# Kernel tuning notes

Hardware: AMD Instinct MI355X
Metric: run time of the kernel (lower is better)

The kernel has to match this reference:

```python
import jax, jax.numpy as jnp
import numpy as np

N_HEAD = 16
N_STATE = 1024
NEG_INF = -1e9


def setup_inputs() -> dict:
    key = jax.random.key(0)
    k1, = jax.random.split(key, 1)
    B, S = 4, 2048
    x = jax.random.normal(k1, (B, S, 3 * N_STATE), dtype=jnp.float32)
    # causal attention mask (1 = keep, 0 = masked), broadcast over heads
    attn_mask = jnp.tril(jnp.ones((S, S), dtype=jnp.float32))[None, None, :, :]
    attn_mask = jnp.broadcast_to(attn_mask, (B, 1, S, S))
    return {"x": x, "attn_mask": attn_mask}


def reference(x, attn_mask) -> jnp.ndarray:
    B, S, _ = x.shape
    d_head = N_STATE // N_HEAD
    q = x[:, :, :N_STATE].reshape(B, S, N_HEAD, d_head).transpose(0, 2, 1, 3)  # [B,H,S,D]
    k = x[:, :, N_STATE:2 * N_STATE].reshape(B, S, N_HEAD, d_head).transpose(0, 2, 1, 3)
    v = x[:, :, 2 * N_STATE:].reshape(B, S, N_HEAD, d_head).transpose(0, 2, 1, 3)
    scale = 1.0 / jnp.sqrt(jnp.asarray(d_head, dtype=x.dtype))
    w = jnp.einsum('bhqd,bhkd->bhqk', q, k) * scale           # [B,H,S,S]
    w = attn_mask * w + (1.0 - attn_mask) * NEG_INF
    w = jax.nn.softmax(w, axis=-1)
    # attention_dropout is identity at inference (Keras Dropout, training=False)
    a = jnp.einsum('bhqk,bhkd->bhqd', w, v)                   # [B,H,S,D]
    return a.transpose(0, 2, 1, 3).reshape(B, S, N_STATE)
```

## Files before the change

### kernel.cpp

```cpp
#include <hip/hip_runtime.h>


typedef float  f32x4  __attribute__((ext_vector_type(4)));
typedef short  bf16x8 __attribute__((ext_vector_type(8)));

#define NH      16
#define DH      64
#define SEQ     2048
#define NSTATE  1024
#define ROW3    3072
#define BQ      128
#define BK      64
#define NQB     (SEQ / BQ)
#define KST     72
#define VST     72
#define PST     72
#define NEG_BIG (-1e9f)
#define QSC     (0.125f * 1.4426950408889634f)

static __device__ __forceinline__ unsigned pk2(float x, float y) {
    unsigned ux = __builtin_bit_cast(unsigned, x);
    unsigned uy = __builtin_bit_cast(unsigned, y);
    ux += 0x7FFFu + ((ux >> 16) & 1u);
    uy += 0x7FFFu + ((uy >> 16) & 1u);
    return __builtin_amdgcn_perm(uy, ux, 0x07060302u);
}

#define ISSUE_STAGE(KV0)                                                       \
    {                                                                          \
        _Pragma("unroll")                                                      \
        for (int i = 0; i < 2; ++i) {                                          \
            int p  = tid + 512 * i;                                            \
            int kv = p >> 4;                                                   \
            int d  = (p & 15) * 4;                                             \
            kp[i] = *(const float4*)(kbase + (size_t)((KV0) + kv) * ROW3 + d); \
        }                                                                      \
        _Pragma("unroll")                                                      \
        for (int i = 0; i < 4; ++i) {                                          \
            int idx = tid + 512 * i;                                           \
            int d   = idx & 63;                                                \
            int kv  = (idx >> 6) * 2;                                          \
            const float* gp = vbase + (size_t)((KV0) + kv) * ROW3 + d;         \
            vp[2 * i]     = gp[0];                                             \
            vp[2 * i + 1] = gp[ROW3];                                          \
        }                                                                      \
    }

#define COMMIT_STAGE(BUF)                                                      \
    {                                                                          \
        _Pragma("unroll")                                                      \
        for (int i = 0; i < 2; ++i) {                                          \
            int p  = tid + 512 * i;                                            \
            int kv = p >> 4;                                                   \
            int d  = (p & 15) * 4;                                             \
            uint2 w;                                                           \
            w.x = pk2(kp[i].x, kp[i].y);                                       \
            w.y = pk2(kp[i].z, kp[i].w);                                       \
            *(uint2*)&Klds[BUF][kv * KST + d] = w;                             \
        }                                                                      \
        _Pragma("unroll")                                                      \
        for (int i = 0; i < 4; ++i) {                                          \
            int idx = tid + 512 * i;                                           \
            int d   = idx & 63;                                                \
            int kv  = (idx >> 6) * 2;                                          \
            *(unsigned*)&Vlds[BUF][d * VST + kv] = pk2(vp[2 * i], vp[2 * i + 1]); \
        }                                                                      \
    }

__global__ __launch_bounds__(512, 4)
void mha_fwd(const float* __restrict__ x, float* __restrict__ out) {
    const int tid  = threadIdx.x;
    const int wave = tid >> 6;
    const int lane = tid & 63;
    const int l16  = lane & 15;
    const int quad = lane >> 4;

    const int pr = blockIdx.x;
    const int bh = blockIdx.y;
    const int b  = bh >> 4;
    const int h  = bh & 15;

    const float* xb    = x + (size_t)b * SEQ * ROW3;
    const float* kbase = xb + NSTATE + h * DH;
    const float* vbase = xb + 2 * NSTATE + h * DH;
    float*       ob    = out + (size_t)b * SEQ * NSTATE + h * DH;

    __shared__ __align__(16) short Klds[2][BK * KST];
    __shared__ __align__(16) short Vlds[2][DH * VST];
    __shared__ __align__(16) short Plds[8][16 * PST];

    bf16x8 vones;
#pragma unroll
    for (int i = 0; i < 8; ++i) vones[i] = (short)0x3F80;

    float4 kp[2];
    float  vp[8];

#pragma unroll 1
    for (int ph = 0; ph < 2; ++ph) {
        const int qblk = ph ? (NQB - 1 - pr) : pr;
        const int q0   = qblk * BQ;
        const int qmin = q0 + wave * 16;
        const int qrow = qmin + l16;

        bf16x8 qf[2];
        {
            const float* qp = xb + (size_t)qrow * ROW3 + h * DH + quad * 8;
#pragma unroll
            for (int f = 0; f < 2; ++f) {
                float4 a = *(const float4*)(qp + 32 * f);
                float4 c = *(const float4*)(qp + 32 * f + 4);
                union { bf16x8 v; unsigned u[4]; } qq;
                qq.u[0] = pk2(a.x * QSC, a.y * QSC);
                qq.u[1] = pk2(a.z * QSC, a.w * QSC);
                qq.u[2] = pk2(c.x * QSC, c.y * QSC);
                qq.u[3] = pk2(c.z * QSC, c.w * QSC);
                qf[f] = qq.v;
            }
        }

        f32x4 o[4];
#pragma unroll
        for (int t = 0; t < 4; ++t) o[t] = (f32x4){0.f, 0.f, 0.f, 0.f};
        f32x4 ol = (f32x4){0.f, 0.f, 0.f, 0.f};

        const int ntiles = q0 / BK + BQ / BK;

        __syncthreads();
        ISSUE_STAGE(0)
        COMMIT_STAGE(0)
        __syncthreads();

#pragma unroll 1
        for (int it = 0; it < ntiles; ++it) {
            const int kv0 = it * BK;
            const int cur = it & 1;
            const bool pf = (it + 1 < ntiles);

            if (pf) ISSUE_STAGE((it + 1) * BK)

            if (kv0 <= qmin + 15) {
                bf16x8 kf[4][2];
#pragma unroll
                for (int t = 0; t < 4; ++t)
#pragma unroll
                    for (int f = 0; f < 2; ++f)
                        kf[t][f] = *(const bf16x8*)&Klds[cur][(16 * t + l16) * KST + quad * 8 + 32 * f];
                bf16x8 vf[4][2];
#pragma unroll
                for (int t = 0; t < 4; ++t)
#pragma unroll
                    for (int f = 0; f < 2; ++f)
                        vf[t][f] = *(const bf16x8*)&Vlds[cur][(16 * t + l16) * VST + quad * 8 + 32 * f];

                f32x4 sc[4];
#pragma unroll
                for (int t = 0; t < 4; ++t) {
                    f32x4 c = (f32x4){0.f, 0.f, 0.f, 0.f};
                    c = __builtin_amdgcn_mfma_f32_16x16x32_bf16(kf[t][0], qf[0], c, 0, 0, 0);
                    c = __builtin_amdgcn_mfma_f32_16x16x32_bf16(kf[t][1], qf[1], c, 0, 0, 0);
                    sc[t] = c;
                }
                if (kv0 + BK - 1 > qmin) {
#pragma unroll
                    for (int t = 0; t < 4; ++t)
#pragma unroll
                        for (int r = 0; r < 4; ++r) {
                            int kvg = kv0 + 16 * t + 4 * quad + r;
                            if (kvg > qrow) sc[t][r] = NEG_BIG;
                        }
                }

#pragma unroll
                for (int t = 0; t < 4; ++t)
#pragma unroll
                    for (int r = 0; r < 4; ++r)
                        sc[t][r] = __builtin_amdgcn_exp2f(sc[t][r]);

                short* pb = &Plds[wave][0];
#pragma unroll
                for (int t = 0; t < 4; ++t) {
                    uint2 pk;
                    pk.x = pk2(sc[t][0], sc[t][1]);
                    pk.y = pk2(sc[t][2], sc[t][3]);
                    *(uint2*)&pb[l16 * PST + 16 * t + 4 * quad] = pk;
                }
                __asm__ volatile("s_waitcnt lgkmcnt(0)" ::: "memory");
                bf16x8 pf0 = *(const bf16x8*)&pb[l16 * PST + quad * 8];
                bf16x8 pf1 = *(const bf16x8*)&pb[l16 * PST + quad * 8 + 32];

#pragma unroll
                for (int t = 0; t < 4; ++t) {
                    f32x4 c = o[t];
                    c = __builtin_amdgcn_mfma_f32_16x16x32_bf16(pf0, vf[t][0], c, 0, 0, 0);
                    c = __builtin_amdgcn_mfma_f32_16x16x32_bf16(pf1, vf[t][1], c, 0, 0, 0);
                    o[t] = c;
                }
                ol = __builtin_amdgcn_mfma_f32_16x16x32_bf16(pf0, vones, ol, 0, 0, 0);
                ol = __builtin_amdgcn_mfma_f32_16x16x32_bf16(pf1, vones, ol, 0, 0, 0);
            }

            if (pf) COMMIT_STAGE(cur ^ 1)
            __syncthreads();
        }

        {
            const int qtop = qmin + 4 * quad;
            float lr[4];
#pragma unroll
            for (int r = 0; r < 4; ++r) lr[r] = 1.0f / ol[r];
#pragma unroll
            for (int t = 0; t < 4; ++t)
#pragma unroll
                for (int r = 0; r < 4; ++r)
                    ob[(size_t)(qtop + r) * NSTATE + 16 * t + l16] = o[t][r] * lr[r];
        }
    }
}

extern "C" void kernel_launch(void* const* d_in, const int* in_sizes, int n_in,
                              void* d_out, int out_size, void* d_ws, size_t ws_size,
                              hipStream_t stream) {
    const float* x = (const float*)d_in[0];
    float* out = (float*)d_out;
    dim3 grid(NQB / 2, 4 * NH);
    dim3 block(512);
    hipLaunchKernelGGL(mha_fwd, grid, block, 0, stream, x, out);
}
```

Measured before the change: 252.7 us.

## Switch attention to 32x32x16 MFMA with register-resident P and larger Q tiles

Replaces the 16x16x32 MFMA tiles with 32x32x16 MFMAs, so each wave owns a 32-row query strip and the query block grows to 256. The P matrix is now repacked in registers with v_permlane32_swap instead of going through an LDS round trip. The row sum is accumulated with VALU adds rather than an extra ones-MFMA, and the grid is flattened so blocks sharing a query block are grouped by head. In exchange, the larger tiles raise register pressure and the launch bounds drop to 2 blocks per SM. With only 4 paired blocks per head, there are fewer workgroups overall.

After: 219.1 us. -13.3%, faster.

```diff
diff --git a/kernel.cpp b/kernel.cpp
--- a/kernel.cpp
+++ b/kernel.cpp
@@ -1,20 +1,20 @@
 #include <hip/hip_runtime.h>
 
 
-typedef float  f32x4  __attribute__((ext_vector_type(4)));
-typedef short  bf16x8 __attribute__((ext_vector_type(8)));
+typedef float  f32x4   __attribute__((ext_vector_type(4)));
+typedef float  f32x16  __attribute__((ext_vector_type(16)));
+typedef short  bf16x8  __attribute__((ext_vector_type(8)));
 
 #define NH      16
 #define DH      64
 #define SEQ     2048
 #define NSTATE  1024
 #define ROW3    3072
-#define BQ      128
+#define BQ      256
 #define BK      64
 #define NQB     (SEQ / BQ)
 #define KST     72
 #define VST     72
-#define PST     72
 #define NEG_BIG (-1e9f)
 #define QSC     (0.125f * 1.4426950408889634f)
 
@@ -33,13 +33,12 @@
             int p  = tid + 512 * i;                                            \
             int kv = p >> 4;                                                   \
             int d  = (p & 15) * 4;                                             \
-            kp[i] = *(const float4*)(kbase + (size_t)((KV0) + kv) * ROW3 + d); \
+            kp[i] = *(const f32x4*)(kbase + (size_t)((KV0) + kv) * ROW3 + d);  \
         }                                                                      \
         _Pragma("unroll")                                                      \
         for (int i = 0; i < 4; ++i) {                                          \
-            int idx = tid + 512 * i;                                           \
-            int d   = idx & 63;                                                \
-            int kv  = (idx >> 6) * 2;                                          \
+            int d  = (tid & 15) + 16 * i;                                      \
+            int kv = (tid >> 4) * 2;                                           \
             const float* gp = vbase + (size_t)((KV0) + kv) * ROW3 + d;         \
             vp[2 * i]     = gp[0];                                             \
             vp[2 * i + 1] = gp[ROW3];                                          \
@@ -54,31 +53,31 @@
             int kv = p >> 4;                                                   \
             int d  = (p & 15) * 4;                                             \
             uint2 w;                                                           \
-            w.x = pk2(kp[i].x, kp[i].y);                                       \
-            w.y = pk2(kp[i].z, kp[i].w);                                       \
+            w.x = pk2(kp[i][0], kp[i][1]);                                     \
+            w.y = pk2(kp[i][2], kp[i][3]);                                     \
             *(uint2*)&Klds[BUF][kv * KST + d] = w;                             \
         }                                                                      \
         _Pragma("unroll")                                                      \
         for (int i = 0; i < 4; ++i) {                                          \
-            int idx = tid + 512 * i;                                           \
-            int d   = idx & 63;                                                \
-            int kv  = (idx >> 6) * 2;                                          \
+            int d  = (tid & 15) + 16 * i;                                      \
+            int kv = (tid >> 4) * 2;                                           \
             *(unsigned*)&Vlds[BUF][d * VST + kv] = pk2(vp[2 * i], vp[2 * i + 1]); \
         }                                                                      \
     }
 
-__global__ __launch_bounds__(512, 4)
+__global__ __launch_bounds__(512, 2)
 void mha_fwd(const float* __restrict__ x, float* __restrict__ out) {
     const int tid  = threadIdx.x;
     const int wave = tid >> 6;
     const int lane = tid & 63;
-    const int l16  = lane & 15;
-    const int quad = lane >> 4;
-
-    const int pr = blockIdx.x;
-    const int bh = blockIdx.y;
-    const int b  = bh >> 4;
-    const int h  = bh & 15;
+    const int r31  = lane & 31;
+    const int hl   = lane >> 5;
+
+    const int bid = blockIdx.x;
+    const int pr  = bid >> 6;
+    const int bh  = bid & 63;
+    const int b   = bh >> 4;
+    const int h   = bh & 15;
 
     const float* xb    = x + (size_t)b * SEQ * ROW3;
     const float* kbase = xb + NSTATE + h * DH;
@@ -87,42 +86,37 @@
 
     __shared__ __align__(16) short Klds[2][BK * KST];
     __shared__ __align__(16) short Vlds[2][DH * VST];
-    __shared__ __align__(16) short Plds[8][16 * PST];
-
-    bf16x8 vones;
-#pragma unroll
-    for (int i = 0; i < 8; ++i) vones[i] = (short)0x3F80;
-
-    float4 kp[2];
-    float  vp[8];
+
+    f32x4 kp[2];
+    float vp[8];
 
 #pragma unroll 1
     for (int ph = 0; ph < 2; ++ph) {
-        const int qblk = ph ? (NQB - 1 - pr) : pr;
-        const int q0   = qblk * BQ;
-        const int qmin = q0 + wave * 16;
-        const int qrow = qmin + l16;
-
-        bf16x8 qf[2];
+        const int qblk   = ph ? (NQB - 1 - pr) : pr;
+        const int q0     = qblk * BQ;
+        const int qstrip = q0 + wave * 32;
+        const int qrow   = qstrip + r31;
+
+        bf16x8 qf[4];
         {
-            const float* qp = xb + (size_t)qrow * ROW3 + h * DH + quad * 8;
-#pragma unroll
-            for (int f = 0; f < 2; ++f) {
-                float4 a = *(const float4*)(qp + 32 * f);
-                float4 c = *(const float4*)(qp + 32 * f + 4);
+            const float* qp = xb + (size_t)qrow * ROW3 + h * DH + hl * 8;
+#pragma unroll
+            for (int kc = 0; kc < 4; ++kc) {
+                f32x4 a = *(const f32x4*)(qp + 16 * kc);
+                f32x4 c = *(const f32x4*)(qp + 16 * kc + 4);
                 union { bf16x8 v; unsigned u[4]; } qq;
-                qq.u[0] = pk2(a.x * QSC, a.y * QSC);
-                qq.u[1] = pk2(a.z * QSC, a.w * QSC);
-                qq.u[2] = pk2(c.x * QSC, c.y * QSC);
-                qq.u[3] = pk2(c.z * QSC, c.w * QSC);
-                qf[f] = qq.v;
+                qq.u[0] = pk2(a[0] * QSC, a[1] * QSC);
+                qq.u[1] = pk2(a[2] * QSC, a[3] * QSC);
+                qq.u[2] = pk2(c[0] * QSC, c[1] * QSC);
+                qq.u[3] = pk2(c[2] * QSC, c[3] * QSC);
+                qf[kc] = qq.v;
             }
         }
 
-        f32x4 o[4];
-#pragma unroll
-        for (int t = 0; t < 4; ++t) o[t] = (f32x4){0.f, 0.f, 0.f, 0.f};
-        f32x4 ol = (f32x4){0.f, 0.f, 0.f, 0.f};
+        f32x16 o0, o1;
+#pragma unroll
+        for (int r = 0; r < 16; ++r) { o0[r] = 0.f; o1[r] = 0.f; }
+        float dl = 0.f;
 
         const int ntiles = q0 / BK + BQ / BK;
 
@@ -139,65 +133,63 @@
 
             if (pf) ISSUE_STAGE((it + 1) * BK)
 
-            if (kv0 <= qmin + 15) {
-                bf16x8 kf[4][2];
-#pragma unroll
-                for (int t = 0; t < 4; ++t)
-#pragma unroll
-                    for (int f = 0; f < 2; ++f)
-                        kf[t][f] = *(const bf16x8*)&Klds[cur][(16 * t + l16) * KST + quad * 8 + 32 * f];
-                bf16x8 vf[4][2];
-#pragma unroll
-                for (int t = 0; t < 4; ++t)
-#pragma unroll
-                    for (int f = 0; f < 2; ++f)
-                        vf[t][f] = *(const bf16x8*)&Vlds[cur][(16 * t + l16) * VST + quad * 8 + 32 * f];
-
-                f32x4 sc[4];
-#pragma unroll
-                for (int t = 0; t < 4; ++t) {
-                    f32x4 c = (f32x4){0.f, 0.f, 0.f, 0.f};
-                    c = __builtin_amdgcn_mfma_f32_16x16x32_bf16(kf[t][0], qf[0], c, 0, 0, 0);
-                    c = __builtin_amdgcn_mfma_f32_16x16x32_bf16(kf[t][1], qf[1], c, 0, 0, 0);
-                    sc[t] = c;
+            if (kv0 <= qstrip + 31) {
+#pragma unroll
+                for (int H = 0; H < 2; ++H) {
+                    const int kvb = kv0 + 32 * H;
+                    if (kvb <= qstrip + 31) {
+                        bf16x8 kf[4];
+#pragma unroll
+                        for (int kc = 0; kc < 4; ++kc)
+                            kf[kc] = *(const bf16x8*)&Klds[cur][(32 * H + r31) * KST + 16 * kc + 8 * hl];
+
+                        f32x16 s;
+#pragma unroll
+                        for (int r = 0; r < 16; ++r) s[r] = 0.f;
+#pragma unroll
+                        for (int kc = 0; kc < 4; ++kc)
+                            s = __builtin_amdgcn_mfma_f32_32x32x16_bf16(kf[kc], qf[kc], s, 0, 0, 0);
+
+                        if (kvb + 31 > qstrip) {
+#pragma unroll
+                            for (int r = 0; r < 16; ++r) {
+                                int kvg = kvb + (r & 3) + 8 * (r >> 2) + 4 * hl;
+                                if (kvg > qrow) s[r] = NEG_BIG;
+                            }
+                        }
+#pragma unroll
+                        for (int r = 0; r < 16; ++r)
+                            s[r] = __builtin_amdgcn_exp2f(s[r]);
+
+                        {
+                            float a0 = (s[0] + s[1]) + (s[2] + s[3]);
+                            float a1 = (s[4] + s[5]) + (s[6] + s[7]);
+                            float a2 = (s[8] + s[9]) + (s[10] + s[11]);
+                            float a3 = (s[12] + s[13]) + (s[14] + s[15]);
+                            dl += (a0 + a1) + (a2 + a3);
+                        }
+
+#pragma unroll
+                        for (int cc = 0; cc < 2; ++cc) {
+                            unsigned wA = pk2(s[8 * cc + 0], s[8 * cc + 1]);
+                            unsigned wB = pk2(s[8 * cc + 2], s[8 * cc + 3]);
+                            unsigned wC = pk2(s[8 * cc + 4], s[8 * cc + 5]);
+                            unsigned wD = pk2(s[8 * cc + 6], s[8 * cc + 7]);
+                            __asm__ volatile("v_permlane32_swap_b32 %0, %1"
+                                             : "+v"(wA), "+v"(wC));
+                            __asm__ volatile("v_permlane32_swap_b32 %0, %1"
+                                             : "+v"(wB), "+v"(wD));
+                            union { bf16x8 v; unsigned u[4]; } pa;
+                            pa.u[0] = wA; pa.u[1] = wB; pa.u[2] = wC; pa.u[3] = wD;
+
+                            const int c = 2 * H + cc;
+                            bf16x8 vf0 = *(const bf16x8*)&Vlds[cur][(r31)      * VST + 16 * c + 8 * hl];
+                            bf16x8 vf1 = *(const bf16x8*)&Vlds[cur][(32 + r31) * VST + 16 * c + 8 * hl];
+                            o0 = __builtin_amdgcn_mfma_f32_32x32x16_bf16(pa.v, vf0, o0, 0, 0, 0);
+                            o1 = __builtin_amdgcn_mfma_f32_32x32x16_bf16(pa.v, vf1, o1, 0, 0, 0);
+                        }
+                    }
                 }
-                if (kv0 + BK - 1 > qmin) {
-#pragma unroll
-                    for (int t = 0; t < 4; ++t)
-#pragma unroll
-                        for (int r = 0; r < 4; ++r) {
-                            int kvg = kv0 + 16 * t + 4 * quad + r;
-                            if (kvg > qrow) sc[t][r] = NEG_BIG;
-                        }
-                }
-
-#pragma unroll
-                for (int t = 0; t < 4; ++t)
-#pragma unroll
-                    for (int r = 0; r < 4; ++r)
-                        sc[t][r] = __builtin_amdgcn_exp2f(sc[t][r]);
-
-                short* pb = &Plds[wave][0];
-#pragma unroll
-                for (int t = 0; t < 4; ++t) {
-                    uint2 pk;
-                    pk.x = pk2(sc[t][0], sc[t][1]);
-                    pk.y = pk2(sc[t][2], sc[t][3]);
-                    *(uint2*)&pb[l16 * PST + 16 * t + 4 * quad] = pk;
-                }
-                __asm__ volatile("s_waitcnt lgkmcnt(0)" ::: "memory");
-                bf16x8 pf0 = *(const bf16x8*)&pb[l16 * PST + quad * 8];
-                bf16x8 pf1 = *(const bf16x8*)&pb[l16 * PST + quad * 8 + 32];
-
-#pragma unroll
-                for (int t = 0; t < 4; ++t) {
-                    f32x4 c = o[t];
-                    c = __builtin_amdgcn_mfma_f32_16x16x32_bf16(pf0, vf[t][0], c, 0, 0, 0);
-                    c = __builtin_amdgcn_mfma_f32_16x16x32_bf16(pf1, vf[t][1], c, 0, 0, 0);
-                    o[t] = c;
-                }
-                ol = __builtin_amdgcn_mfma_f32_16x16x32_bf16(pf0, vones, ol, 0, 0, 0);
-                ol = __builtin_amdgcn_mfma_f32_16x16x32_bf16(pf1, vones, ol, 0, 0, 0);
             }
 
             if (pf) COMMIT_STAGE(cur ^ 1)
@@ -205,15 +197,21 @@
         }
 
         {
-            const int qtop = qmin + 4 * quad;
-            float lr[4];
-#pragma unroll
-            for (int r = 0; r < 4; ++r) lr[r] = 1.0f / ol[r];
-#pragma unroll
-            for (int t = 0; t < 4; ++t)
-#pragma unroll
-                for (int r = 0; r < 4; ++r)
-                    ob[(size_t)(qtop + r) * NSTATE + 16 * t + l16] = o[t][r] * lr[r];
+            unsigned da = __builtin_bit_cast(unsigned, dl);
+            unsigned db = da;
+            __asm__ volatile("v_permlane32_swap_b32 %0, %1" : "+v"(da), "+v"(db));
+            float dtot = __builtin_bit_cast(float, da) + __builtin_bit_cast(float, db);
+            float rcp  = 1.0f / dtot;
+#pragma unroll
+            for (int r = 0; r < 16; ++r) {
+                int srcq = (r & 3) + 8 * (r >> 2) + 4 * hl;
+                float lr = __builtin_bit_cast(float,
+                    __builtin_amdgcn_ds_bpermute(srcq << 2,
+                        __builtin_bit_cast(int, rcp)));
+                const size_t row = (size_t)(qstrip + srcq) * NSTATE;
+                ob[row + r31]      = o0[r] * lr;
+                ob[row + 32 + r31] = o1[r] * lr;
+            }
         }
     }
 }
@@ -223,7 +221,7 @@
                               hipStream_t stream) {
     const float* x = (const float*)d_in[0];
     float* out = (float*)d_out;
-    dim3 grid(NQB / 2, 4 * NH);
+    dim3 grid(4 * NH * (NQB / 2));
     dim3 block(512);
     hipLaunchKernelGGL(mha_fwd, grid, block, 0, stream, x, out);
 }
```
